# Kernel optimization log

Measured on AMD Instinct MI355X. Metric: run time of the kernel, lower is better.

## Reference

```python
import jax, jax.numpy as jnp
import numpy as np

HH = 38  # sqrt(amd0=1444)
KD = 3   # 3x3 neighborhood


def setup_inputs() -> dict:
    key = jax.random.key(0)
    fm = jax.random.normal(key, (16, 512, HH, HH), dtype=jnp.float32)
    return {"fm": fm}


def reference(fm):
    # fm: [B, C, H, W] -> replication pad 1 -> NHWC -> gather 3x3 neighbors,
    # concatenated along the channel axis in row-major neighbor order
    # (matching counts[:, 0..8] = (h-1,w-1),(h-1,w),(h-1,w+1),(h,w-1),...).
    B, C, H, W = fm.shape
    x = jnp.pad(fm, ((0, 0), (0, 0), (1, 1), (1, 1)), mode="edge")  # [B,C,H+2,W+2]
    x = jnp.transpose(x, (0, 2, 3, 1))  # [B, H+2, W+2, C]
    patches = [x[:, di:di + H, dj:dj + W, :] for di in range(KD) for dj in range(KD)]
    pfm = jnp.concatenate(patches, axis=-1)  # [B, H, W, 9*C]
    return pfm.reshape(B, H * W, KD * KD * C)  # [B, 1444, 9*C]
```

## Files before the change

kernel.cpp:

```cpp
#include <hip/hip_runtime.h>


#define BB 16
#define CC 512
#define HH 38
#define WW 38
#define HW (HH * WW)
#define KK 9
#define NT 512

__global__ __launch_bounds__(NT) void spatial_pool_scatter(
    const float* __restrict__ fm, float* __restrict__ out)
{
    const int bh = blockIdx.x;
    const int h  = bh % HH;
    const int b  = bh / HH;
    const int c  = threadIdx.x;

    const float* src = fm + ((size_t)(b * CC + c)) * HW + h * WW;
    float v[WW];
    #pragma unroll
    for (int i = 0; i < WW / 2; ++i) {
        const float2 r = *((const float2*)src + i);
        v[2 * i + 0] = r.x;
        v[2 * i + 1] = r.y;
    }

    int hrow[3];
    {
        int n = 0;
        #pragma unroll
        for (int di = 0; di < 3; ++di) {
            int hm = h + 1 - di;
            if (0 <= hm && hm < HH) { hrow[n] = (b * HW + hm * WW) * KK + di * 3; n++; }
        }
        if (h == 0)      { hrow[n] = (b * HW) * KK; n++; }
        if (h == HH - 1) { hrow[n] = (b * HW + (HH - 1) * WW) * KK + 6; n++; }
    }

    float* outc = out + c;
    #pragma unroll
    for (int w = 0; w < WW; ++w) {
        int woff[3];
        int m = 0;
        #pragma unroll
        for (int dj = 0; dj < 3; ++dj) {
            int wm = w + 1 - dj;
            if (0 <= wm && wm < WW) { woff[m] = wm * KK + dj; m++; }
        }
        if (w == 0)      { woff[m] = 0; m++; }
        if (w == WW - 1) { woff[m] = (WW - 1) * KK + 2; m++; }
        const float val = v[w];
        #pragma unroll
        for (int i = 0; i < 3; ++i) {
            #pragma unroll
            for (int j = 0; j < 3; ++j) {
                unsigned idx = (unsigned)(hrow[i] + woff[j]) * (unsigned)CC;
                __builtin_nontemporal_store(val, outc + (size_t)idx);
            }
        }
    }
}

extern "C" void kernel_launch(void* const* d_in, const int* in_sizes, int n_in,
                              void* d_out, int out_size, void* d_ws, size_t ws_size,
                              hipStream_t stream) {
    const float* fm = (const float*)d_in[0];
    float* out = (float*)d_out;
    dim3 grid(BB * HH);
    dim3 block(NT);
    spatial_pool_scatter<<<grid, block, 0, stream>>>(fm, out);
}
```

Measured before the change: 451.6 us.

## Switch scatter to gather per output row half with XCD-aware block mapping

Each block now owns one output row half (19 pixels) and gathers the three input rows it needs, instead of each input row scattering to up to nine output rows. Output writes for a block become a contiguous region, which should improve write locality. Block indices are remapped so each XCD handles a fixed set of batches, and the grid doubles to give more parallelism. In exchange each input row is read about three times, and the per-thread register array grows to 60 floats.

```diff
diff --git a/kernel.cpp b/kernel.cpp
--- a/kernel.cpp
+++ b/kernel.cpp
@@ -9,57 +9,66 @@
 #define KK 9
 #define NT 512
 
-__global__ __launch_bounds__(NT) void spatial_pool_scatter(
-    const float* __restrict__ fm, float* __restrict__ out)
+template <int HALF>
+__device__ __forceinline__ void do_half(const float* __restrict__ fm,
+                                        float* __restrict__ out,
+                                        int b, int hp, int c)
 {
-    const int bh = blockIdx.x;
-    const int h  = bh % HH;
-    const int b  = bh / HH;
-    const int c  = threadIdx.x;
+    constexpr int W0 = HALF * 19;
+    constexpr int WN = 19;
+    constexpr int WA = HALF * 18;
+    constexpr int NL = 10;
 
-    const float* src = fm + ((size_t)(b * CC + c)) * HW + h * WW;
-    float v[WW];
+    const int r0 = (hp > 0) ? hp - 1 : 0;
+    const int r2 = (hp < HH - 1) ? hp + 1 : HH - 1;
+    const int rows[3] = { r0, hp, r2 };
+
+    const float* plane = fm + (size_t)(b * CC + c) * HW;
+
+    float v[3][2 * NL];
     #pragma unroll
-    for (int i = 0; i < WW / 2; ++i) {
-        const float2 r = *((const float2*)src + i);
-        v[2 * i + 0] = r.x;
-        v[2 * i + 1] = r.y;
+    for (int di = 0; di < 3; ++di) {
+        const float2* src = (const float2*)(plane + rows[di] * WW + WA);
+        #pragma unroll
+        for (int i = 0; i < NL; ++i) {
+            const float2 t = src[i];
+            v[di][2 * i + 0] = t.x;
+            v[di][2 * i + 1] = t.y;
+        }
     }
 
-    int hrow[3];
-    {
-        int n = 0;
+    float* outp = out + (size_t)((b * HW + hp * WW + W0) * KK) * CC + c;
+    #pragma unroll
+    for (int wi = 0; wi < WN; ++wi) {
         #pragma unroll
         for (int di = 0; di < 3; ++di) {
-            int hm = h + 1 - di;
-            if (0 <= hm && hm < HH) { hrow[n] = (b * HW + hm * WW) * KK + di * 3; n++; }
-        }
-        if (h == 0)      { hrow[n] = (b * HW) * KK; n++; }
-        if (h == HH - 1) { hrow[n] = (b * HW + (HH - 1) * WW) * KK + 6; n++; }
-    }
-
-    float* outc = out + c;
-    #pragma unroll
-    for (int w = 0; w < WW; ++w) {
-        int woff[3];
-        int m = 0;
-        #pragma unroll
-        for (int dj = 0; dj < 3; ++dj) {
-            int wm = w + 1 - dj;
-            if (0 <= wm && wm < WW) { woff[m] = wm * KK + dj; m++; }
-        }
-        if (w == 0)      { woff[m] = 0; m++; }
-        if (w == WW - 1) { woff[m] = (WW - 1) * KK + 2; m++; }
-        const float val = v[w];
-        #pragma unroll
-        for (int i = 0; i < 3; ++i) {
             #pragma unroll
-            for (int j = 0; j < 3; ++j) {
-                unsigned idx = (unsigned)(hrow[i] + woff[j]) * (unsigned)CC;
-                __builtin_nontemporal_store(val, outc + (size_t)idx);
+            for (int dj = 0; dj < 3; ++dj) {
+                int wj = W0 + wi + dj - 1;
+                wj = wj < 0 ? 0 : (wj > WW - 1 ? WW - 1 : wj);
+                __builtin_nontemporal_store(
+                    v[di][wj - WA],
+                    outp + (size_t)(wi * KK + di * 3 + dj) * CC);
             }
         }
     }
+}
+
+__global__ __launch_bounds__(NT) void spatial_pool_gather(
+    const float* __restrict__ fm, float* __restrict__ out)
+{
+    const unsigned L = blockIdx.x;
+    const int xcd  = (int)(L & 7u);
+    const int slot = (int)(L >> 3);
+    const int bsel = slot / 76;
+    const int rem  = slot - bsel * 76;
+    const int hp   = rem >> 1;
+    const int half = rem & 1;
+    const int b    = xcd + 8 * bsel;
+    const int c    = (int)threadIdx.x;
+
+    if (half == 0) do_half<0>(fm, out, b, hp, c);
+    else           do_half<1>(fm, out, b, hp, c);
 }
 
 extern "C" void kernel_launch(void* const* d_in, const int* in_sizes, int n_in,
@@ -67,7 +76,7 @@
                               hipStream_t stream) {
     const float* fm = (const float*)d_in[0];
     float* out = (float*)d_out;
-    dim3 grid(BB * HH);
+    dim3 grid(BB * HH * 2);
     dim3 block(NT);
-    spatial_pool_scatter<<<grid, block, 0, stream>>>(fm, out);
+    spatial_pool_gather<<<grid, block, 0, stream>>>(fm, out);
 }
```

Result: slower. 463.2 us (+2.6%).

## Vectorize scatter stores to float4 across channels and split rows into quarters

Applied to the files above, without the earlier changes.

Each thread now handles 4 consecutive channels and writes 16-byte nontemporal vector stores instead of scalar stores. The width dimension is split into four chunks handled by separate blocks, and block size drops to 128 threads, which quadruples the grid and shrinks per-thread register arrays. The intent is to cut the number of store instructions and raise occupancy and parallelism. The cost is that loads now come from four strided channel planes per thread, so reads are less coalesced.

```diff
diff --git a/kernel.cpp b/kernel.cpp
--- a/kernel.cpp
+++ b/kernel.cpp
@@ -7,25 +7,16 @@
 #define WW 38
 #define HW (HH * WW)
 #define KK 9
-#define NT 512
+#define NT 128
 
-__global__ __launch_bounds__(NT) void spatial_pool_scatter(
-    const float* __restrict__ fm, float* __restrict__ out)
+typedef float f32x2 __attribute__((ext_vector_type(2)));
+typedef float f32x4 __attribute__((ext_vector_type(4)));
+
+template <int W0, int WN>
+__device__ __forceinline__ void do_q(const float* __restrict__ fm,
+                                     float* __restrict__ out,
+                                     int b, int h, int c0)
 {
-    const int bh = blockIdx.x;
-    const int h  = bh % HH;
-    const int b  = bh / HH;
-    const int c  = threadIdx.x;
-
-    const float* src = fm + ((size_t)(b * CC + c)) * HW + h * WW;
-    float v[WW];
-    #pragma unroll
-    for (int i = 0; i < WW / 2; ++i) {
-        const float2 r = *((const float2*)src + i);
-        v[2 * i + 0] = r.x;
-        v[2 * i + 1] = r.y;
-    }
-
     int hrow[3];
     {
         int n = 0;
@@ -38,27 +29,62 @@
         if (h == HH - 1) { hrow[n] = (b * HW + (HH - 1) * WW) * KK + 6; n++; }
     }
 
-    float* outc = out + c;
+    const float* p0 = fm + (size_t)(b * CC + c0 + 0) * HW + h * WW + W0;
+    const float* p1 = p0 + HW;
+    const float* p2 = p0 + 2 * HW;
+    const float* p3 = p0 + 3 * HW;
+    float* ob = out + c0;
+
     #pragma unroll
-    for (int w = 0; w < WW; ++w) {
-        int woff[3];
-        int m = 0;
+    for (int i2 = 0; i2 < WN / 2; ++i2) {
+        const f32x2 t0 = *(const f32x2*)(p0 + 2 * i2);
+        const f32x2 t1 = *(const f32x2*)(p1 + 2 * i2);
+        const f32x2 t2 = *(const f32x2*)(p2 + 2 * i2);
+        const f32x2 t3 = *(const f32x2*)(p3 + 2 * i2);
+        const f32x4 va = (f32x4){t0.x, t1.x, t2.x, t3.x};
+        const f32x4 vb = (f32x4){t0.y, t1.y, t2.y, t3.y};
+
         #pragma unroll
-        for (int dj = 0; dj < 3; ++dj) {
-            int wm = w + 1 - dj;
-            if (0 <= wm && wm < WW) { woff[m] = wm * KK + dj; m++; }
-        }
-        if (w == 0)      { woff[m] = 0; m++; }
-        if (w == WW - 1) { woff[m] = (WW - 1) * KK + 2; m++; }
-        const float val = v[w];
-        #pragma unroll
-        for (int i = 0; i < 3; ++i) {
+        for (int par = 0; par < 2; ++par) {
+            const int w = W0 + 2 * i2 + par;
+            const f32x4 val = par ? vb : va;
+            int woff[3];
+            int m = 0;
             #pragma unroll
-            for (int j = 0; j < 3; ++j) {
-                unsigned idx = (unsigned)(hrow[i] + woff[j]) * (unsigned)CC;
-                __builtin_nontemporal_store(val, outc + (size_t)idx);
+            for (int dj = 0; dj < 3; ++dj) {
+                int wm = w + 1 - dj;
+                if (0 <= wm && wm < WW) { woff[m] = wm * KK + dj; m++; }
+            }
+            if (w == 0)      { woff[m] = 0; m++; }
+            if (w == WW - 1) { woff[m] = (WW - 1) * KK + 2; m++; }
+
+            #pragma unroll
+            for (int i = 0; i < 3; ++i) {
+                #pragma unroll
+                for (int j = 0; j < 3; ++j) {
+                    const unsigned idx = (unsigned)(hrow[i] + woff[j]) * (unsigned)CC;
+                    __builtin_nontemporal_store(val, (f32x4*)(ob + (size_t)idx));
+                }
             }
         }
+    }
+}
+
+__global__ __launch_bounds__(NT) void spatial_pool_stream(
+    const float* __restrict__ fm, float* __restrict__ out)
+{
+    const unsigned L = blockIdx.x;
+    const int q  = (int)(L / 608u);
+    const int bh = (int)(L - 608u * q);
+    const int h  = bh % HH;
+    const int b  = bh / HH;
+    const int c0 = 4 * (int)threadIdx.x;
+
+    switch (q) {
+        case 0:  do_q< 0, 10>(fm, out, b, h, c0); break;
+        case 1:  do_q<10, 10>(fm, out, b, h, c0); break;
+        case 2:  do_q<20, 10>(fm, out, b, h, c0); break;
+        default: do_q<30,  8>(fm, out, b, h, c0); break;
     }
 }
 
@@ -67,7 +93,7 @@
                               hipStream_t stream) {
     const float* fm = (const float*)d_in[0];
     float* out = (float*)d_out;
-    dim3 grid(BB * HH);
+    dim3 grid(BB * HH * 4);
     dim3 block(NT);
-    spatial_pool_scatter<<<grid, block, 0, stream>>>(fm, out);
+    spatial_pool_stream<<<grid, block, 0, stream>>>(fm, out);
 }
```

Result: no change. 449.2 us (-0.5%).

## Vectorize scatter stores over four channels and retile grid by channel groups and row chunks

Applied to the files above, without the earlier changes.

Each thread now handles four consecutive channels and two adjacent pixels, loading float2 from four channel planes and issuing 16-byte nontemporal stores for each of the nine neighbor slots. The grid is split by batch, 32-channel group and 5-row chunk, giving many more smaller blocks. The aim is fewer store instructions and better occupancy in this write-bound scatter. In exchange, each wave's stores are split across 128-byte segments, and loads are strided across channel planes.

```diff
diff --git a/kernel.cpp b/kernel.cpp
--- a/kernel.cpp
+++ b/kernel.cpp
@@ -7,56 +7,71 @@
 #define WW 38
 #define HW (HH * WW)
 #define KK 9
-#define NT 512
+#define NT 256
+#define CG 32
+#define HC 5
 
-__global__ __launch_bounds__(NT) void spatial_pool_scatter(
+typedef float f32x2 __attribute__((ext_vector_type(2)));
+typedef float f32x4 __attribute__((ext_vector_type(4)));
+
+__global__ __launch_bounds__(NT) void spatial_pool_closure(
     const float* __restrict__ fm, float* __restrict__ out)
 {
-    const int bh = blockIdx.x;
-    const int h  = bh % HH;
-    const int b  = bh / HH;
-    const int c  = threadIdx.x;
+    const unsigned L = blockIdx.x;
+    const int hc  = (int)(L & 7u);
+    const int cgb = (int)((L >> 3) & 15u);
+    const int b   = (int)(L >> 7);
 
-    const float* src = fm + ((size_t)(b * CC + c)) * HW + h * WW;
-    float v[WW];
-    #pragma unroll
-    for (int i = 0; i < WW / 2; ++i) {
-        const float2 r = *((const float2*)src + i);
-        v[2 * i + 0] = r.x;
-        v[2 * i + 1] = r.y;
-    }
+    const int R0 = hc * HC;
+    const int NR = (hc == 7) ? (HH - R0) : HC;
+    const int NP = NR * 19;
 
-    int hrow[3];
-    {
-        int n = 0;
+    const int t  = (int)threadIdx.x;
+    const int c4 = t & 7;
+    const int pp = t >> 3;
+
+    const int c0 = cgb * CG + 4 * c4;
+    const float* pl0 = fm + (size_t)(b * CC + c0) * HW;
+    float* ob = out + c0;
+    const int obase = b * HW;
+
+    for (int p = pp; p < NP; p += 32) {
+        const int lr  = p / 19;
+        const int wp  = p - lr * 19;
+        const int h   = R0 + lr;
+        const int w0  = 2 * wp;
+
+        const size_t ro = (size_t)h * WW + w0;
+        const f32x2 t0 = *(const f32x2*)(pl0 + (size_t)0 * HW + ro);
+        const f32x2 t1 = *(const f32x2*)(pl0 + (size_t)1 * HW + ro);
+        const f32x2 t2 = *(const f32x2*)(pl0 + (size_t)2 * HW + ro);
+        const f32x2 t3 = *(const f32x2*)(pl0 + (size_t)3 * HW + ro);
+        const f32x4 va = (f32x4){t0.x, t1.x, t2.x, t3.x};
+        const f32x4 vb = (f32x4){t0.y, t1.y, t2.y, t3.y};
+
+        const int hr0 = (h < HH - 1) ? (obase + (h + 1) * WW) * KK + 0
+                                     : (obase + (HH - 1) * WW) * KK + 6;
+        const int hr1 = (obase + h * WW) * KK + 3;
+        const int hr2 = (h > 0) ? (obase + (h - 1) * WW) * KK + 6
+                                : (obase) * KK + 0;
+
         #pragma unroll
-        for (int di = 0; di < 3; ++di) {
-            int hm = h + 1 - di;
-            if (0 <= hm && hm < HH) { hrow[n] = (b * HW + hm * WW) * KK + di * 3; n++; }
-        }
-        if (h == 0)      { hrow[n] = (b * HW) * KK; n++; }
-        if (h == HH - 1) { hrow[n] = (b * HW + (HH - 1) * WW) * KK + 6; n++; }
-    }
+        for (int par = 0; par < 2; ++par) {
+            const int w = w0 + par;
+            const f32x4 val = par ? vb : va;
+            const int wo0 = (w < WW - 1) ? (w + 1) * KK + 0 : (WW - 1) * KK + 2;
+            const int wo1 = w * KK + 1;
+            const int wo2 = (w > 0) ? (w - 1) * KK + 2 : 0;
+            const int wt[3] = { wo0, wo1, wo2 };
+            const int ht[3] = { hr0, hr1, hr2 };
 
-    float* outc = out + c;
-    #pragma unroll
-    for (int w = 0; w < WW; ++w) {
-        int woff[3];
-        int m = 0;
-        #pragma unroll
-        for (int dj = 0; dj < 3; ++dj) {
-            int wm = w + 1 - dj;
-            if (0 <= wm && wm < WW) { woff[m] = wm * KK + dj; m++; }
-        }
-        if (w == 0)      { woff[m] = 0; m++; }
-        if (w == WW - 1) { woff[m] = (WW - 1) * KK + 2; m++; }
-        const float val = v[w];
-        #pragma unroll
-        for (int i = 0; i < 3; ++i) {
             #pragma unroll
-            for (int j = 0; j < 3; ++j) {
-                unsigned idx = (unsigned)(hrow[i] + woff[j]) * (unsigned)CC;
-                __builtin_nontemporal_store(val, outc + (size_t)idx);
+            for (int i = 0; i < 3; ++i) {
+                #pragma unroll
+                for (int j = 0; j < 3; ++j) {
+                    const unsigned idx = (unsigned)(ht[i] + wt[j]) * (unsigned)CC;
+                    __builtin_nontemporal_store(val, (f32x4*)(ob + (size_t)idx));
+                }
             }
         }
     }
@@ -67,7 +82,7 @@
                               hipStream_t stream) {
     const float* fm = (const float*)d_in[0];
     float* out = (float*)d_out;
-    dim3 grid(BB * HH);
+    dim3 grid(BB * (CC / CG) * 8);
     dim3 block(NT);
-    spatial_pool_scatter<<<grid, block, 0, stream>>>(fm, out);
+    spatial_pool_closure<<<grid, block, 0, stream>>>(fm, out);
 }
```

After: 456.9 us. No clear change (+1.2%).
